# Optimization experiments

Measured on AMD Instinct MI355X. Metric: run time of the kernel, lower is better.

Reference implementation:

```python
import jax, jax.numpy as jnp
import numpy as np

T, B, OBS, HID = 64, 1024, 8, 512
N_ODE_STEPS = 4  # fixed-step RK4 over t in [0, 1]
LN_EPS = 1e-5


def _ln(x, g, b):
    m = x.mean(-1, keepdims=True)
    v = ((x - m) ** 2).mean(-1, keepdims=True)
    return (x - m) / jnp.sqrt(v + LN_EPS) * g + b


def setup_inputs() -> dict:
    key = jax.random.key(0)
    ks = jax.random.split(key, 24)

    def w(k, shape, fan_in):
        s = 1.0 / np.sqrt(fan_in)
        return jax.random.uniform(k, shape, jnp.float32, -s, s)

    return {
        "xs": jax.random.normal(ks[0], (T, B, OBS), jnp.float32),
        # obs2hidden MLP: Linear + LayerNorm + LeakyReLU
        "obs_W": w(ks[1], (OBS, HID), OBS),
        "obs_b": w(ks[2], (HID,), OBS),
        "obs_ln_g": jnp.ones((HID,), jnp.float32),
        "obs_ln_b": jnp.zeros((HID,), jnp.float32),
        # ODE func MLP (time-concat input, 2 hidden layers, linear out)
        "ode_W1": w(ks[3], (HID + 1, HID), HID + 1),
        "ode_b1": w(ks[4], (HID,), HID + 1),
        "ode_ln1_g": jnp.ones((HID,), jnp.float32),
        "ode_ln1_b": jnp.zeros((HID,), jnp.float32),
        "ode_W2": w(ks[5], (HID, HID), HID),
        "ode_b2": w(ks[6], (HID,), HID),
        "ode_ln2_g": jnp.ones((HID,), jnp.float32),
        "ode_ln2_b": jnp.zeros((HID,), jnp.float32),
        "ode_Wout": w(ks[7], (HID, HID), HID),
        "ode_bout": w(ks[8], (HID,), HID),
        # GRU cell (torch gate order: r, z, n)
        "W_ih": w(ks[9], (HID, 3 * HID), HID),
        "b_ih": w(ks[10], (3 * HID,), HID),
        "W_hh": w(ks[11], (HID, 3 * HID), HID),
        "b_hh": w(ks[12], (3 * HID,), HID),
    }


def reference(xs, obs_W, obs_b, obs_ln_g, obs_ln_b,
              ode_W1, ode_b1, ode_ln1_g, ode_ln1_b,
              ode_W2, ode_b2, ode_ln2_g, ode_ln2_b,
              ode_Wout, ode_bout, W_ih, b_ih, W_hh, b_hh):
    batch = xs.shape[1]

    # obs -> hidden for all timesteps at once: [T, B, HID]
    hs = jax.nn.leaky_relu(_ln(xs @ obs_W + obs_b, obs_ln_g, obs_ln_b))

    def ode_f(h, t):  # h: [B, HID], t: scalar
        ht = jnp.concatenate([h, jnp.full((batch, 1), t, h.dtype)], axis=-1)
        z = jax.nn.leaky_relu(_ln(ht @ ode_W1 + ode_b1, ode_ln1_g, ode_ln1_b))
        z = jax.nn.leaky_relu(_ln(z @ ode_W2 + ode_b2, ode_ln2_g, ode_ln2_b))
        return z @ ode_Wout + ode_bout

    dt = 1.0 / N_ODE_STEPS

    def rk4_solve(h0):
        def body(h, t):
            k1 = ode_f(h, t)
            k2 = ode_f(h + 0.5 * dt * k1, t + 0.5 * dt)
            k3 = ode_f(h + 0.5 * dt * k2, t + 0.5 * dt)
            k4 = ode_f(h + dt * k3, t + dt)
            return h + (dt / 6.0) * (k1 + 2 * k2 + 2 * k3 + k4), None
        ts = jnp.arange(N_ODE_STEPS, dtype=h0.dtype) * dt
        h, _ = jax.lax.scan(body, h0, ts)
        return h

    def gru_cell(x, h):
        gi = x @ W_ih + b_ih
        gh = h @ W_hh + b_hh
        i_r, i_z, i_n = jnp.split(gi, 3, axis=-1)
        h_r, h_z, h_n = jnp.split(gh, 3, axis=-1)
        r = jax.nn.sigmoid(i_r + h_r)
        z = jax.nn.sigmoid(i_z + h_z)
        n = jnp.tanh(i_n + r * h_n)
        return (1.0 - z) * n + z * h

    def step(h_prev, h_obs):
        h_ode = rk4_solve(h_obs)          # NeuralODE: integrate from t=0 to 1
        h_new = gru_cell(h_ode, h_prev)   # GRU step
        return h_new, None

    h0 = jnp.zeros((batch, hs.shape[-1]), hs.dtype)
    h_final, _ = jax.lax.scan(step, h0, hs)
    return h_final  # [B, HID]
```

## Files before the change

### kernel.cpp

```cpp
#include <hip/hip_runtime.h>
#include <stdint.h>


typedef __bf16 bf16x8 __attribute__((ext_vector_type(8)));
typedef float floatx4 __attribute__((ext_vector_type(4)));

#define BP 40
#define KSR 257
#define REDW 9

static __device__ __forceinline__ float bf2f(unsigned short u) {
  union { unsigned int u32; float f; } c;
  c.u32 = ((unsigned int)u) << 16;
  return c.f;
}
static __device__ __forceinline__ unsigned short f2bf(float f) {
  union { __bf16 h; unsigned short u; } c;
  c.h = (__bf16)f;
  return c.u;
}
static __device__ __forceinline__ unsigned int pk2(float a, float b) {
  return (unsigned int)f2bf(a) | ((unsigned int)f2bf(b) << 16);
}

static __device__ __forceinline__ void barrier_lds() {
  __asm__ volatile("s_waitcnt lgkmcnt(0)\n\ts_barrier" ::: "memory");
}

__global__ void tile_weight(const float* __restrict__ src, unsigned short* __restrict__ dst) {
  int t = blockIdx.x * 256 + threadIdx.x;
  int ml = t & 15, qd = (t >> 4) & 3;
  int nt = (t >> 6) & 31, kk = t >> 11;
  int n = nt * 16 + ml;
  int k0 = kk * 32 + qd * 8;
  unsigned short o[8] __attribute__((aligned(16)));
#pragma unroll
  for (int j = 0; j < 8; ++j) o[j] = f2bf(src[(size_t)(k0 + j) * 512 + n]);
  *(uint4*)(dst + (size_t)t * 8) = *(const uint4*)o;
}

__global__ void transpose_f2b(const float* __restrict__ src, unsigned short* __restrict__ dst,
                              int R, int C) {
  __shared__ float t[32][33];
  int c0 = blockIdx.x * 32, r0 = blockIdx.y * 32;
  int tx = threadIdx.x, ty = threadIdx.y;
#pragma unroll
  for (int i = 0; i < 32; i += 8) t[ty + i][tx] = src[(size_t)(r0 + ty + i) * C + c0 + tx];
  __syncthreads();
#pragma unroll
  for (int i = 0; i < 32; i += 8) dst[(size_t)(c0 + ty + i) * R + r0 + tx] = f2bf(t[tx][ty + i]);
}

__global__ __launch_bounds__(256) void obs_embed(
    const float* __restrict__ xs, const float* __restrict__ W,
    const float* __restrict__ bias, const float* __restrict__ gam,
    const float* __restrict__ bet, unsigned short* __restrict__ Y) {
  __shared__ float Wl[4096];
  const int tid = threadIdx.x, lane = tid & 63, wv = tid >> 6;
#pragma unroll
  for (int i = 0; i < 16; ++i) Wl[i * 256 + tid] = W[i * 256 + tid];
  __syncthreads();
  size_t row = (size_t)blockIdx.x * 4 + wv;
  float xf[8];
  {
    const float* xp = xs + row * 8;
#pragma unroll
    for (int k = 0; k < 8; ++k) xf[k] = xp[k];
  }
  int n0 = lane * 8;
  float a[8];
#pragma unroll
  for (int j = 0; j < 8; ++j) a[j] = bias[n0 + j];
#pragma unroll
  for (int k = 0; k < 8; ++k)
#pragma unroll
    for (int j = 0; j < 8; ++j) a[j] += xf[k] * Wl[k * 512 + n0 + j];
  float s1 = 0.f, s2 = 0.f;
#pragma unroll
  for (int j = 0; j < 8; ++j) { s1 += a[j]; s2 += a[j] * a[j]; }
#pragma unroll
  for (int off = 1; off < 64; off <<= 1) { s1 += __shfl_xor(s1, off); s2 += __shfl_xor(s2, off); }
  float mean = s1 * (1.f / 512.f);
  float rstd = rsqrtf(s2 * (1.f / 512.f) - mean * mean + 1e-5f);
  unsigned short o[8] __attribute__((aligned(16)));
#pragma unroll
  for (int j = 0; j < 8; ++j) {
    float v = (a[j] - mean) * rstd * gam[n0 + j] + bet[n0 + j];
    v = v > 0.f ? v : 0.01f * v;
    o[j] = f2bf(v);
  }
  *(uint4*)(Y + row * 512 + n0) = *(const uint4*)o;
}


static __device__ __forceinline__ int a_addr(int row, int n) {
  return (((row >> 4) * 16 + (n >> 5)) * 4 + ((n >> 3) & 3)) * 128 + (row & 15) * 8 + (n & 7);
}

static __device__ __forceinline__ void bload(const unsigned short* __restrict__ Wt, int kk,
                                             int wvoff, bf16x8 (&b)[4]) {
  const unsigned short* p = Wt + (size_t)kk * 16384 + wvoff;
#pragma unroll
  for (int j = 0; j < 4; ++j) b[j] = *(const bf16x8*)(p + j * 512);
}

static __device__ __forceinline__ void gemmS(const unsigned short* __restrict__ Wt,
                                             const unsigned short* __restrict__ Wnext,
                                             const unsigned short* As, int wvoff, int lane,
                                             const floatx4 (&bias)[4],
                                             bf16x8 (&bb)[2][4], floatx4 (&acc)[4][4]) {
#pragma unroll
  for (int mi = 0; mi < 4; ++mi)
#pragma unroll
    for (int j = 0; j < 4; ++j) acc[mi][j] = bias[j];
#pragma unroll 2
  for (int kk = 0; kk < 16; ++kk) {
#pragma unroll
    for (int mh = 0; mh < 2; ++mh) {
      bf16x8 a0 = *(const bf16x8*)&As[((2 * mh) * 16 + kk) * 512 + lane * 8];
      bf16x8 a1 = *(const bf16x8*)&As[((2 * mh + 1) * 16 + kk) * 512 + lane * 8];
#pragma unroll
      for (int j = 0; j < 4; ++j) {
        acc[2 * mh][j] =
            __builtin_amdgcn_mfma_f32_16x16x32_bf16(bb[kk & 1][j], a0, acc[2 * mh][j], 0, 0, 0);
        acc[2 * mh + 1][j] =
            __builtin_amdgcn_mfma_f32_16x16x32_bf16(bb[kk & 1][j], a1, acc[2 * mh + 1][j], 0, 0, 0);
      }
    }
    if (kk < 14) bload(Wt, kk + 2, wvoff, bb[kk & 1]);
    else bload(Wnext, kk - 14, wvoff, bb[kk & 1]);
  }
}

static __device__ __forceinline__ void ln_epi(floatx4 (&acc)[4][4], unsigned short* As,
                                              const float* Pg, const float* Pb,
                                              int wv, int lane, float2* red) {
  const int ml = lane & 15, qd = lane >> 4;
#pragma unroll
  for (int mi = 0; mi < 4; ++mi) {
    float s1 = 0.f, s2 = 0.f;
#pragma unroll
    for (int j = 0; j < 4; ++j)
#pragma unroll
      for (int r = 0; r < 4; ++r) { float x = acc[mi][j][r]; s1 += x; s2 += x * x; }
    s1 += __shfl_xor(s1, 16); s2 += __shfl_xor(s2, 16);
    s1 += __shfl_xor(s1, 32); s2 += __shfl_xor(s2, 32);
    if (qd == 0) red[(mi * 16 + ml) * REDW + wv] = make_float2(s1, s2);
  }
  barrier_lds();
  float mean[4], rstd[4];
#pragma unroll
  for (int mi = 0; mi < 4; ++mi) {
    float S1 = 0.f, S2 = 0.f;
#pragma unroll
    for (int w = 0; w < 8; ++w) {
      float2 v = red[(mi * 16 + ml) * REDW + w];
      S1 += v.x; S2 += v.y;
    }
    float m = S1 * (1.f / 512.f);
    mean[mi] = m;
    rstd[mi] = rsqrtf(S2 * (1.f / 512.f) - m * m + 1e-5f);
  }
#pragma unroll
  for (int j = 0; j < 4; ++j) {
    int nb = (4 * wv + j) * 16 + qd * 4;
    floatx4 gm = *(const floatx4*)&Pg[nb];
    floatx4 bt = *(const floatx4*)&Pb[nb];
#pragma unroll
    for (int mi = 0; mi < 4; ++mi) {
      float x0 = (acc[mi][j][0] - mean[mi]) * rstd[mi] * gm[0] + bt[0];
      float x1 = (acc[mi][j][1] - mean[mi]) * rstd[mi] * gm[1] + bt[1];
      float x2 = (acc[mi][j][2] - mean[mi]) * rstd[mi] * gm[2] + bt[2];
      float x3 = (acc[mi][j][3] - mean[mi]) * rstd[mi] * gm[3] + bt[3];
      x0 = x0 > 0.f ? x0 : 0.01f * x0;
      x1 = x1 > 0.f ? x1 : 0.01f * x1;
      x2 = x2 > 0.f ? x2 : 0.01f * x2;
      x3 = x3 > 0.f ? x3 : 0.01f * x3;
      uint2 o = make_uint2(pk2(x0, x1), pk2(x2, x3));
      *(uint2*)(As + a_addr(mi * 16 + ml, nb)) = o;
    }
  }
  barrier_lds();
}

static __device__ __forceinline__ void stage_epi(floatx4 (&acc)[4][4], float (&h)[4][4][4],
                                                 unsigned int* Ks, unsigned short* As,
                                                 unsigned short* Yb, size_t m0,
                                                 int stg, bool last, int wv, int lane) {
  const int ml = lane & 15, qd = lane >> 4;
  barrier_lds();
#pragma unroll
  for (int mi = 0; mi < 4; ++mi) {
    int rowK = (mi * 16 + ml) * KSR;
#pragma unroll
    for (int j = 0; j < 4; ++j) {
      int nb = (4 * wv + j) * 16 + qd * 4;
      unsigned int yw[2];
#pragma unroll
      for (int p = 0; p < 2; ++p) {
        int kidx = rowK + (4 * wv + j) * 8 + qd * 2 + p;
        float kv0 = acc[mi][j][2 * p];
        float kv1 = acc[mi][j][2 * p + 1];
        unsigned int pk = (stg != 0) ? Ks[kidx] : 0u;
        float s0 = bf2f((unsigned short)(pk & 0xffffu));
        float s1 = bf2f((unsigned short)(pk >> 16));
        float h0 = h[mi][j][2 * p], h1 = h[mi][j][2 * p + 1];
        float y0, y1;
        if (stg == 0)      { s0 = kv0;        s1 = kv1;        y0 = h0 + 0.125f * kv0; y1 = h1 + 0.125f * kv1; }
        else if (stg == 1) { s0 += 2.f * kv0; s1 += 2.f * kv1; y0 = h0 + 0.125f * kv0; y1 = h1 + 0.125f * kv1; }
        else if (stg == 2) { s0 += 2.f * kv0; s1 += 2.f * kv1; y0 = h0 + 0.25f * kv0;  y1 = h1 + 0.25f * kv1; }
        else {
          h0 += (1.f / 24.f) * (s0 + kv0);
          h1 += (1.f / 24.f) * (s1 + kv1);
          h[mi][j][2 * p] = h0; h[mi][j][2 * p + 1] = h1;
          y0 = h0; y1 = h1;
        }
        if (stg != 3) Ks[kidx] = pk2(s0, s1);
        yw[p] = pk2(y0, y1);
      }
      uint2 o = make_uint2(yw[0], yw[1]);
      *(uint2*)(As + a_addr(mi * 16 + ml, nb)) = o;
      if (last && stg == 3)
        *(uint2*)(Yb + (m0 + mi * 16 + ml) * 512 + nb) = o;
    }
  }
  barrier_lds();
}

__global__ __launch_bounds__(512) void ode_mega(
    unsigned short* Yb, const unsigned short* __restrict__ W1t,
    const unsigned short* __restrict__ W2t, const unsigned short* __restrict__ Wot,
    const float* __restrict__ b1, const float* __restrict__ tr, const float* __restrict__ g1,
    const float* __restrict__ be1, const float* __restrict__ b2, const float* __restrict__ g2,
    const float* __restrict__ be2, const float* __restrict__ bo) {
  __shared__ __align__(16) unsigned short As[32768];
  __shared__ __align__(16) float Pf[8 * 512];
  __shared__ float2 red[64 * REDW];
  __shared__ __align__(16) unsigned int Ks[64 * KSR];

  const int tid = threadIdx.x;
  const int lane = tid & 63;
  const int wv = tid >> 6;
  const int ml = lane & 15;
  const int qd = lane >> 4;
  const size_t m0 = (size_t)blockIdx.x * 64;
  const int wvoff = wv * 2048 + lane * 8;

  bf16x8 bb[2][4];
  bload(W1t, 0, wvoff, bb[0]);
  bload(W1t, 1, wvoff, bb[1]);

  {
    const float* srcs[8] = {b1, tr, g1, be1, b2, g2, be2, bo};
#pragma unroll
    for (int v = 0; v < 8; ++v) Pf[v * 512 + tid] = srcs[v][tid];
  }

  {
    int r = tid >> 3;
    int c0 = tid & 7;
#pragma unroll
    for (int i = 0; i < 8; ++i) {
      int c = c0 + i * 8;
      uint4 v = *(const uint4*)(Yb + (m0 + r) * 512 + c * 8);
      int dst = (((r >> 4) * 16 + (c >> 2)) * 4 + (c & 3)) * 128 + (r & 15) * 8;
      *(uint4*)(As + dst) = v;
    }
  }
  barrier_lds();

  float h[4][4][4];
#pragma unroll
  for (int mi = 0; mi < 4; ++mi)
#pragma unroll
    for (int j = 0; j < 4; ++j) {
      int nb = (4 * wv + j) * 16 + qd * 4;
      uint2 v = *(const uint2*)(As + a_addr(mi * 16 + ml, nb));
      h[mi][j][0] = bf2f((unsigned short)(v.x & 0xffffu));
      h[mi][j][1] = bf2f((unsigned short)(v.x >> 16));
      h[mi][j][2] = bf2f((unsigned short)(v.y & 0xffffu));
      h[mi][j][3] = bf2f((unsigned short)(v.y >> 16));
    }

  for (int e = 0; e < 16; ++e) {
    int stg = e & 3;
    float tval = 0.25f * (float)(e >> 2) + ((stg == 3) ? 0.25f : (stg ? 0.125f : 0.f));
    floatx4 acc[4][4];
    floatx4 bias[4];

#pragma unroll
    for (int j = 0; j < 4; ++j) {
      int nb = (4 * wv + j) * 16 + qd * 4;
      floatx4 vb = *(const floatx4*)&Pf[0 * 512 + nb];
      floatx4 vt = *(const floatx4*)&Pf[1 * 512 + nb];
#pragma unroll
      for (int r = 0; r < 4; ++r) bias[j][r] = vb[r] + tval * vt[r];
    }
    gemmS(W1t, W2t, As, wvoff, lane, bias, bb, acc);
    ln_epi(acc, As, Pf + 2 * 512, Pf + 3 * 512, wv, lane, red);

#pragma unroll
    for (int j = 0; j < 4; ++j) {
      int nb = (4 * wv + j) * 16 + qd * 4;
      bias[j] = *(const floatx4*)&Pf[4 * 512 + nb];
    }
    gemmS(W2t, Wot, As, wvoff, lane, bias, bb, acc);
    ln_epi(acc, As, Pf + 5 * 512, Pf + 6 * 512, wv, lane, red);

#pragma unroll
    for (int j = 0; j < 4; ++j) {
      int nb = (4 * wv + j) * 16 + qd * 4;
      bias[j] = *(const floatx4*)&Pf[7 * 512 + nb];
    }
    gemmS(Wot, W1t, As, wvoff, lane, bias, bb, acc);
    stage_epi(acc, h, Ks, As, Yb, m0, stg, e == 15, wv, lane);
  }
}

__global__ __launch_bounds__(256) void gru_step(
    const unsigned short* __restrict__ Yt, const float* __restrict__ hprev,
    float* __restrict__ hnew, const unsigned short* __restrict__ Wiht,
    const unsigned short* __restrict__ Whht, const float* __restrict__ bih,
    const float* __restrict__ bhh) {
  __shared__ __align__(16) unsigned short Ay[32 * BP];
  __shared__ __align__(16) unsigned short Ah[32 * BP];
  __shared__ __align__(16) unsigned short Bg[6 * 64 * BP];
  const int tid = threadIdx.x, lane = tid & 63, wv = tid >> 6;
  const int ml = lane & 15, qd = lane >> 4;
  const int m0 = blockIdx.x * 32;
  const int j0 = blockIdx.y * 64;

  floatx4 acc[2][6];
#pragma unroll
  for (int mi = 0; mi < 2; ++mi)
#pragma unroll
    for (int g = 0; g < 6; ++g) acc[mi][g] = 0.f;

  for (int kk = 0; kk < 16; ++kk) {
    __syncthreads();
#pragma unroll
    for (int c = 0; c < 7; ++c) {
      int id = c * 256 + tid;
      if (id < 128) {
        int r = id >> 2, kc = id & 3;
        *(uint4*)(Ay + r * BP + kc * 8) =
            *(const uint4*)(Yt + (size_t)(m0 + r) * 512 + kk * 32 + kc * 8);
      } else if (id < 256) {
        int id2 = id - 128;
        int r = id2 >> 2, kc = id2 & 3;
        const float* s = hprev + (size_t)(m0 + r) * 512 + kk * 32 + kc * 8;
        unsigned short o[8] __attribute__((aligned(16)));
#pragma unroll
        for (int j = 0; j < 8; ++j) o[j] = f2bf(s[j]);
        *(uint4*)(Ah + r * BP + kc * 8) = *(const uint4*)o;
      } else {
        int id2 = id - 256;
        int g = id2 >> 8;
        int rem = id2 & 255;
        int r = rem >> 2, kc = rem & 3;
        const unsigned short* mat = (g < 3) ? Wiht : Whht;
        int gate = (g < 3) ? g : (g - 3);
        *(uint4*)(Bg + g * (64 * BP) + r * BP + kc * 8) =
            *(const uint4*)(mat + (size_t)(gate * 512 + j0 + r) * 512 + kk * 32 + kc * 8);
      }
    }
    __syncthreads();
    bf16x8 ay[2], ah[2];
#pragma unroll
    for (int mi = 0; mi < 2; ++mi) {
      ay[mi] = *(const bf16x8*)&Ay[(16 * mi + ml) * BP + qd * 8];
      ah[mi] = *(const bf16x8*)&Ah[(16 * mi + ml) * BP + qd * 8];
    }
#pragma unroll
    for (int g = 0; g < 6; ++g) {
      bf16x8 b = *(const bf16x8*)&Bg[g * (64 * BP) + (16 * wv + ml) * BP + qd * 8];
#pragma unroll
      for (int mi = 0; mi < 2; ++mi)
        acc[mi][g] = __builtin_amdgcn_mfma_f32_16x16x32_bf16((g < 3) ? ay[mi] : ah[mi], b,
                                                             acc[mi][g], 0, 0, 0);
    }
  }
  int j = j0 + 16 * wv + ml;
  float bi_r = bih[j], bi_z = bih[512 + j], bi_n = bih[1024 + j];
  float bh_r = bhh[j], bh_z = bhh[512 + j], bh_n = bhh[1024 + j];
#pragma unroll
  for (int mi = 0; mi < 2; ++mi)
#pragma unroll
    for (int r = 0; r < 4; ++r) {
      size_t row = (size_t)(m0 + 16 * mi + 4 * qd + r);
      float rg = acc[mi][0][r] + bi_r + acc[mi][3][r] + bh_r;
      rg = 1.f / (1.f + __expf(-rg));
      float zg = acc[mi][1][r] + bi_z + acc[mi][4][r] + bh_z;
      zg = 1.f / (1.f + __expf(-zg));
      float ng = tanhf(acc[mi][2][r] + bi_n + rg * (acc[mi][5][r] + bh_n));
      float hp = hprev[row * 512 + j];
      hnew[row * 512 + j] = (1.f - zg) * ng + zg * hp;
    }
}

__global__ void zero_h(float* hf) {
  int i = blockIdx.x * 256 + threadIdx.x;
  hf[i] = 0.f;
}

extern "C" void kernel_launch(void* const* d_in, const int* in_sizes, int n_in,
                              void* d_out, int out_size, void* d_ws, size_t ws_size,
                              hipStream_t stream) {
  (void)in_sizes; (void)n_in; (void)out_size; (void)ws_size;
  const float* xs    = (const float*)d_in[0];
  const float* obsW  = (const float*)d_in[1];
  const float* obsb  = (const float*)d_in[2];
  const float* obsg  = (const float*)d_in[3];
  const float* obsbe = (const float*)d_in[4];
  const float* W1    = (const float*)d_in[5];
  const float* b1    = (const float*)d_in[6];
  const float* g1    = (const float*)d_in[7];
  const float* be1   = (const float*)d_in[8];
  const float* W2    = (const float*)d_in[9];
  const float* b2    = (const float*)d_in[10];
  const float* g2    = (const float*)d_in[11];
  const float* be2   = (const float*)d_in[12];
  const float* Wo    = (const float*)d_in[13];
  const float* bo    = (const float*)d_in[14];
  const float* Wih   = (const float*)d_in[15];
  const float* bih   = (const float*)d_in[16];
  const float* Whh   = (const float*)d_in[17];
  const float* bhh   = (const float*)d_in[18];

  char* p = (char*)d_ws;
  auto take = [&](size_t bytes) { char* q = p; p += (bytes + 255) & ~(size_t)255; return q; };
  unsigned short* W1t  = (unsigned short*)take((size_t)512 * 512 * 2);
  unsigned short* W2t  = (unsigned short*)take((size_t)512 * 512 * 2);
  unsigned short* Wot  = (unsigned short*)take((size_t)512 * 512 * 2);
  unsigned short* Wiht = (unsigned short*)take((size_t)1536 * 512 * 2);
  unsigned short* Whht = (unsigned short*)take((size_t)1536 * 512 * 2);
  float* hf0 = (float*)take((size_t)1024 * 512 * 4);
  float* hf1 = (float*)take((size_t)1024 * 512 * 4);
  unsigned short* Yb = (unsigned short*)take((size_t)65536 * 512 * 2);

  dim3 tb(32, 8);
  tile_weight<<<128, 256, 0, stream>>>(W1, W1t);
  tile_weight<<<128, 256, 0, stream>>>(W2, W2t);
  tile_weight<<<128, 256, 0, stream>>>(Wo, Wot);
  transpose_f2b<<<dim3(48, 16), tb, 0, stream>>>(Wih, Wiht, 512, 1536);
  transpose_f2b<<<dim3(48, 16), tb, 0, stream>>>(Whh, Whht, 512, 1536);

  obs_embed<<<16384, 256, 0, stream>>>(xs, obsW, obsb, obsg, obsbe, Yb);

  ode_mega<<<1024, 512, 0, stream>>>(Yb, W1t, W2t, Wot, b1, W1 + 512 * 512, g1, be1, b2, g2,
                                     be2, bo);

  zero_h<<<2048, 256, 0, stream>>>(hf0);
  float* hf[2] = {hf0, hf1};
  for (int t = 0; t < 64; ++t) {
    int s = t & 1, d = s ^ 1;
    float* hn = (t == 63) ? (float*)d_out : hf[d];
    gru_step<<<dim3(32, 8), 256, 0, stream>>>(Yb + (size_t)t * 1024 * 512, hf[s], hn, Wiht, Whht,
                                              bih, bhh);
  }
}
```

Baseline: 3.280 ms.

## Stage full-K activations in LDS and register-prefetch GRU weights

The GRU step kernel now loads the whole 32x512 Y and h_prev tiles into LDS once, removing the per-k-chunk barriers. Weight fragments are read directly from global memory into registers with a two-deep prefetch ring instead of being staged through LDS. This targets the barrier and LDS-staging overhead of the K loop. In exchange it uses more LDS per block and more registers, which may lower occupancy. Only the GRU kernel changes; the ODE kernel, which likely dominates the runtime, is untouched.

Result: faster. 2.885 ms (-12.1%).

```diff
diff --git a/kernel.cpp b/kernel.cpp
--- a/kernel.cpp
+++ b/kernel.cpp
@@ -5,7 +5,7 @@
 typedef __bf16 bf16x8 __attribute__((ext_vector_type(8)));
 typedef float floatx4 __attribute__((ext_vector_type(4)));
 
-#define BP 40
+#define AP 520
 #define KSR 257
 #define REDW 9
 
@@ -322,64 +322,72 @@
     float* __restrict__ hnew, const unsigned short* __restrict__ Wiht,
     const unsigned short* __restrict__ Whht, const float* __restrict__ bih,
     const float* __restrict__ bhh) {
-  __shared__ __align__(16) unsigned short Ay[32 * BP];
-  __shared__ __align__(16) unsigned short Ah[32 * BP];
-  __shared__ __align__(16) unsigned short Bg[6 * 64 * BP];
+  __shared__ __align__(16) unsigned short Ay[32 * AP];
+  __shared__ __align__(16) unsigned short Ah[32 * AP];
   const int tid = threadIdx.x, lane = tid & 63, wv = tid >> 6;
   const int ml = lane & 15, qd = lane >> 4;
   const int m0 = blockIdx.x * 32;
   const int j0 = blockIdx.y * 64;
 
+  const unsigned short* bp[6];
+#pragma unroll
+  for (int g = 0; g < 6; ++g) {
+    const unsigned short* mat = (g < 3) ? Wiht : Whht;
+    int gate = (g < 3) ? g : (g - 3);
+    bp[g] = mat + (size_t)(gate * 512 + j0 + 16 * wv + ml) * 512 + qd * 8;
+  }
+  bf16x8 bgl[2][6];
+#pragma unroll
+  for (int g = 0; g < 6; ++g) bgl[0][g] = *(const bf16x8*)(bp[g]);
+#pragma unroll
+  for (int g = 0; g < 6; ++g) bgl[1][g] = *(const bf16x8*)(bp[g] + 32);
+
+  {
+    int r = tid >> 3, c0 = tid & 7;
+#pragma unroll
+    for (int i = 0; i < 8; ++i) {
+      int c = c0 + i * 8;
+      *(uint4*)(Ay + r * AP + c * 8) = *(const uint4*)(Yt + (size_t)(m0 + r) * 512 + c * 8);
+    }
+#pragma unroll
+    for (int i = 0; i < 8; ++i) {
+      int c = c0 + i * 8;
+      const float* s = hprev + (size_t)(m0 + r) * 512 + c * 8;
+      unsigned short o[8] __attribute__((aligned(16)));
+#pragma unroll
+      for (int j = 0; j < 8; ++j) o[j] = f2bf(s[j]);
+      *(uint4*)(Ah + r * AP + c * 8) = *(const uint4*)o;
+    }
+  }
+  __syncthreads();
+
   floatx4 acc[2][6];
 #pragma unroll
   for (int mi = 0; mi < 2; ++mi)
 #pragma unroll
     for (int g = 0; g < 6; ++g) acc[mi][g] = 0.f;
 
+#pragma unroll 2
   for (int kk = 0; kk < 16; ++kk) {
-    __syncthreads();
-#pragma unroll
-    for (int c = 0; c < 7; ++c) {
-      int id = c * 256 + tid;
-      if (id < 128) {
-        int r = id >> 2, kc = id & 3;
-        *(uint4*)(Ay + r * BP + kc * 8) =
-            *(const uint4*)(Yt + (size_t)(m0 + r) * 512 + kk * 32 + kc * 8);
-      } else if (id < 256) {
-        int id2 = id - 128;
-        int r = id2 >> 2, kc = id2 & 3;
-        const float* s = hprev + (size_t)(m0 + r) * 512 + kk * 32 + kc * 8;
-        unsigned short o[8] __attribute__((aligned(16)));
-#pragma unroll
-        for (int j = 0; j < 8; ++j) o[j] = f2bf(s[j]);
-        *(uint4*)(Ah + r * BP + kc * 8) = *(const uint4*)o;
-      } else {
-        int id2 = id - 256;
-        int g = id2 >> 8;
-        int rem = id2 & 255;
-        int r = rem >> 2, kc = rem & 3;
-        const unsigned short* mat = (g < 3) ? Wiht : Whht;
-        int gate = (g < 3) ? g : (g - 3);
-        *(uint4*)(Bg + g * (64 * BP) + r * BP + kc * 8) =
-            *(const uint4*)(mat + (size_t)(gate * 512 + j0 + r) * 512 + kk * 32 + kc * 8);
-      }
-    }
-    __syncthreads();
     bf16x8 ay[2], ah[2];
 #pragma unroll
     for (int mi = 0; mi < 2; ++mi) {
-      ay[mi] = *(const bf16x8*)&Ay[(16 * mi + ml) * BP + qd * 8];
-      ah[mi] = *(const bf16x8*)&Ah[(16 * mi + ml) * BP + qd * 8];
+      ay[mi] = *(const bf16x8*)&Ay[(16 * mi + ml) * AP + kk * 32 + qd * 8];
+      ah[mi] = *(const bf16x8*)&Ah[(16 * mi + ml) * AP + kk * 32 + qd * 8];
     }
 #pragma unroll
     for (int g = 0; g < 6; ++g) {
-      bf16x8 b = *(const bf16x8*)&Bg[g * (64 * BP) + (16 * wv + ml) * BP + qd * 8];
 #pragma unroll
       for (int mi = 0; mi < 2; ++mi)
-        acc[mi][g] = __builtin_amdgcn_mfma_f32_16x16x32_bf16((g < 3) ? ay[mi] : ah[mi], b,
-                                                             acc[mi][g], 0, 0, 0);
-    }
-  }
+        acc[mi][g] = __builtin_amdgcn_mfma_f32_16x16x32_bf16((g < 3) ? ay[mi] : ah[mi],
+                                                             bgl[kk & 1][g], acc[mi][g], 0, 0, 0);
+    }
+    if (kk < 14) {
+#pragma unroll
+      for (int g = 0; g < 6; ++g) bgl[kk & 1][g] = *(const bf16x8*)(bp[g] + (kk + 2) * 32);
+    }
+  }
+
   int j = j0 + 16 * wv + ml;
   float bi_r = bih[j], bi_z = bih[512 + j], bi_n = bih[1024 + j];
   float bh_r = bhh[j], bh_z = bhh[512 + j], bh_n = bhh[1024 + j];
```
